# Kernel optimization log

Hardware: AMD Instinct MI355X
Metric: run time of the kernel (lower is better)

## Reference

```python
import jax, jax.numpy as jnp
import numpy as np

NUM_MIXTURES = 10
DIM_INPUT = 512
DIM_FEATURES = 512
SEQ_LEN = 512
BATCH = 16
NUM_CHAR = 1024
DIM_CONTEXT = 256


def setup_inputs() -> dict:
    key = jax.random.key(0)
    ks = jax.random.split(key, 6)
    inputs = jax.random.normal(ks[0], (SEQ_LEN, BATCH, DIM_INPUT), dtype=jnp.float32)
    context_vectors = jax.random.normal(ks[1], (NUM_CHAR, BATCH, DIM_CONTEXT), dtype=jnp.float32)
    init_means = jnp.zeros((BATCH, NUM_MIXTURES), dtype=jnp.float32)
    # StackedLinearLayers params: 2 layers, leaky_relu between, out dim = 3*K
    s1 = 1.0 / np.sqrt(DIM_INPUT)
    s2 = 1.0 / np.sqrt(DIM_FEATURES)
    W1 = jax.random.uniform(ks[2], (DIM_INPUT, DIM_FEATURES), jnp.float32, -s1, s1)
    b1 = jax.random.uniform(ks[3], (DIM_FEATURES,), jnp.float32, -s1, s1)
    W2 = jax.random.uniform(ks[4], (DIM_FEATURES, 3 * NUM_MIXTURES), jnp.float32, -s2, s2)
    b2 = jax.random.uniform(ks[5], (3 * NUM_MIXTURES,), jnp.float32, -s2, s2)
    return dict(inputs=inputs, context_vectors=context_vectors, init_means=init_means,
                W1=W1, b1=b1, W2=W2, b2=b2, extra_chars=0)


def reference(inputs, context_vectors, init_means, W1, b1, W2, b2, extra_chars):
    K = NUM_MIXTURES
    seq_len, batch, _ = inputs.shape
    num_char = context_vectors.shape[0]
    total_char = num_char + extra_chars

    # StackedLinearLayers: leaky_relu MLP, last layer linear -> (S, B, 3K)
    h = jax.nn.leaky_relu(inputs @ W1 + b1, negative_slope=0.01)
    outs = h @ W2 + b2
    outs = jax.nn.softplus(outs)  # pos_fun = softplus

    delta_means, vars_, weights = jnp.split(outs, 3, axis=2)  # each (S, B, K)
    delta_means = delta_means / 25.0
    vars_ = jnp.clip(vars_, 0.01, 100.0)
    means = jnp.cumsum(delta_means, axis=0) + init_means[None, :, :]  # (S, B, K)

    cidxs = jnp.arange(total_char, dtype=jnp.float32)  # (T,)
    # dists: (S, B, K, T)
    dists = -((means[..., None] - cidxs) ** 2) * vars_[..., None]
    # attn_weights = exp(logsumexp over mixtures)
    attn_weights = jnp.exp(
        jax.scipy.special.logsumexp(jnp.log(weights)[..., None] + dists, axis=2)
    )  # (S, B, T)

    # attended contexts: (S, B, D)
    attn_contexts = jnp.einsum('sbc,cbd->sbd', attn_weights[:, :, :num_char], context_vectors)
    return attn_contexts, attn_weights, means, vars_, weights
```

## Files before the change

### kernel.cpp

```cpp
#include <hip/hip_runtime.h>
#include <math.h>

#define S_LEN 512
#define BATCH 16
#define DIN   512
#define DF    512
#define NMIX  10
#define NCHAR 1024
#define DCTX  256
#define M_ROWS (S_LEN*BATCH)

#define OFF_CTXOUT 0
#define OFF_ATTN   (S_LEN*BATCH*DCTX)
#define OFF_MEANS  (OFF_ATTN + S_LEN*BATCH*NCHAR)
#define OFF_VARS   (OFF_MEANS + S_LEN*BATCH*NMIX)
#define OFF_WTS    (OFF_VARS  + S_LEN*BATCH*NMIX)

#define WS_XH    0
#define WS_W1T   (8u<<20)
#define WS_W2T   (9u<<20)
#define WS_HH    (10u<<20)
#define WS_ATTNH (26u<<20)
#define WS_BOUND (44u<<20)

#define NX4     1048576
#define CVT_BLOCKS (NX4/256)
#define W1T_BLOCKS 64
#define W2T_BLOCKS 64

typedef float    f32x16 __attribute__((ext_vector_type(16)));
typedef float    f32x4v __attribute__((ext_vector_type(4)));
typedef _Float16 f16x8  __attribute__((ext_vector_type(8)));

__device__ __forceinline__ unsigned short f2h(float x) {
    union { _Float16 h; unsigned short u; } cv;
    cv.h = (_Float16)x;
    return cv.u;
}
__device__ __forceinline__ ushort4 cvt4(float4 v) {
    ushort4 o; o.x = f2h(v.x); o.y = f2h(v.y); o.z = f2h(v.z); o.w = f2h(v.w);
    return o;
}
__device__ __forceinline__ void nt_store4(float* p, float a, float b, float c, float d) {
    f32x4v v; v.x = a; v.y = b; v.z = c; v.w = d;
    __builtin_nontemporal_store(v, (f32x4v*)p);
}

__global__ __launch_bounds__(256) void convert_kernel(
    const float* __restrict__ X, const float* __restrict__ W1,
    const float* __restrict__ W2,
    unsigned short* __restrict__ Xh, unsigned short* __restrict__ W1T,
    float* __restrict__ W2T, unsigned int* __restrict__ bound)
{
    const int bid = blockIdx.x;
    const int tid = threadIdx.x;
    if (bid < CVT_BLOCKS) {
        const int i4 = bid*256 + tid;
        ((ushort4*)Xh)[i4] = cvt4(((const float4*)X)[i4]);
    } else if (bid < CVT_BLOCKS + W1T_BLOCKS) {
        __shared__ unsigned short tile[64*68];
        const int b2 = bid - CVT_BLOCKS;
        const int k0 = (b2 >> 3) * 64, n0 = (b2 & 7) * 64;
        #pragma unroll
        for (int q = 0; q < 4; q++) {
            const int r = q*16 + (tid >> 4);
            const int c = (tid & 15) * 4;
            float4 v = *(const float4*)(W1 + (size_t)(k0+r)*DF + n0 + c);
            *(ushort4*)(tile + r*68 + c) = cvt4(v);
        }
        __syncthreads();
        #pragma unroll
        for (int q = 0; q < 4; q++) {
            const int n  = q*16 + (tid >> 4);
            const int kq = (tid & 15) * 4;
            ushort4 o;
            o.x = tile[(kq+0)*68 + n];
            o.y = tile[(kq+1)*68 + n];
            o.z = tile[(kq+2)*68 + n];
            o.w = tile[(kq+3)*68 + n];
            *(ushort4*)(W1T + (size_t)(n0+n)*DIN + k0 + kq) = o;
        }
    } else if (bid < CVT_BLOCKS + W1T_BLOCKS + W2T_BLOCKS) {
        const int idx = (bid - CVT_BLOCKS - W1T_BLOCKS)*256 + tid;
        if (idx < 512*32) {
            const int j = idx >> 9, k = idx & 511;
            W2T[idx] = (j < 30) ? W2[k*30 + j] : 0.f;
        }
    } else {
        if (tid < BATCH) bound[tid] = 0u;
    }
}

__global__ __launch_bounds__(256) void gemm1_kernel(
    const unsigned short* __restrict__ Xh, const unsigned short* __restrict__ W1T,
    const float* __restrict__ b1, unsigned short* __restrict__ Hh)
{
    __shared__ __align__(16) unsigned short As[64*72];
    __shared__ __align__(16) unsigned short Bs[64*72];
    const int row0 = (blockIdx.x >> 3) * 64;
    const int n0   = (blockIdx.x & 7)  * 64;
    const int tid  = threadIdx.x;
    const int lane = tid & 63, w = tid >> 6;
    const int wr = (w >> 1) * 32, wc = (w & 1) * 32;
    const int m  = lane & 31,  g  = lane >> 5;
    const int sa = tid >> 2,   ka = (tid & 3) * 16;

    f32x16 acc = {};
    const unsigned short* aptr = Xh  + (size_t)(row0+sa)*DIN + ka;
    const unsigned short* bptr = W1T + (size_t)(n0 +sa)*DIN + ka;

    for (int kt = 0; kt < DIN; kt += 64) {
        uint4 av0 = *(const uint4*)(aptr + kt);
        uint4 av1 = *(const uint4*)(aptr + kt + 8);
        uint4 bv0 = *(const uint4*)(bptr + kt);
        uint4 bv1 = *(const uint4*)(bptr + kt + 8);
        __syncthreads();
        *(uint4*)(As + sa*72 + ka)     = av0;
        *(uint4*)(As + sa*72 + ka + 8) = av1;
        *(uint4*)(Bs + sa*72 + ka)     = bv0;
        *(uint4*)(Bs + sa*72 + ka + 8) = bv1;
        __syncthreads();
        #pragma unroll
        for (int ks = 0; ks < 64; ks += 16) {
            f16x8 af = *(const f16x8*)(As + (wr+m)*72 + ks + g*8);
            f16x8 bf = *(const f16x8*)(Bs + (wc+m)*72 + ks + g*8);
            acc = __builtin_amdgcn_mfma_f32_32x32x16_f16(af, bf, acc, 0, 0, 0);
        }
    }
    const int ncol = n0 + wc + m;
    const float bb = b1[ncol];
    #pragma unroll
    for (int r = 0; r < 16; r++) {
        const int rowloc = (r & 3) + 8*(r >> 2) + 4*g;
        const int row = row0 + wr + rowloc;
        float v = acc[r] + bb;
        v = v > 0.f ? v : 0.01f * v;
        Hh[(size_t)row*DF + ncol] = f2h(v);
    }
}

__global__ __launch_bounds__(256) void gemm2_kernel(
    const unsigned short* __restrict__ Hh, const float* __restrict__ W2T,
    const float* __restrict__ b2,
    float* __restrict__ dmeans, float* __restrict__ dvars, float* __restrict__ dwts)
{
    __shared__ __align__(16) unsigned short Hs[32*520];
    const int tid = threadIdx.x;
    const int r0  = blockIdx.x * 32;
    {
        const uint4* src = (const uint4*)(Hh + (size_t)r0*DF);
        #pragma unroll
        for (int i = 0; i < 8; i++) {
            int u   = tid + i*256;
            int row = u >> 6;
            int col = (u & 63) * 8;
            *(uint4*)(Hs + row*520 + col) = src[u];
        }
    }
    __syncthreads();

    const int r  = tid & 31;
    const int j0 = tid >> 5;
    const unsigned short* hrow = Hs + r*520;
    float acc[4] = {0.f, 0.f, 0.f, 0.f};

    for (int k0 = 0; k0 < DF; k0 += 8) {
        union { uint4 u; _Float16 h[8]; } hv;
        hv.u = *(const uint4*)(hrow + k0);
        float wv[4][8];
        #pragma unroll
        for (int q = 0; q < 4; q++) {
            *(float4*)(wv[q])     = *(const float4*)(W2T + (size_t)(j0 + q*8)*DF + k0);
            *(float4*)(wv[q] + 4) = *(const float4*)(W2T + (size_t)(j0 + q*8)*DF + k0 + 4);
        }
        #pragma unroll
        for (int i = 0; i < 8; i++) {
            float hf = (float)hv.h[i];
            acc[0] = fmaf(hf, wv[0][i], acc[0]);
            acc[1] = fmaf(hf, wv[1][i], acc[1]);
            acc[2] = fmaf(hf, wv[2][i], acc[2]);
            acc[3] = fmaf(hf, wv[3][i], acc[3]);
        }
    }
    const int row = r0 + r;
    #pragma unroll
    for (int q = 0; q < 4; q++) {
        const int j = j0 + q*8;
        if (j >= 30) continue;
        float dot = acc[q] + b2[j];
        float sp  = fmaxf(dot, 0.f) + log1pf(__expf(-fabsf(dot)));
        if (j < 10)       dmeans[row*NMIX + j]      = sp / 25.0f;
        else if (j < 20)  dvars [row*NMIX + (j-10)] = fminf(fmaxf(sp, 0.01f), 100.f);
        else              dwts  [row*NMIX + (j-20)] = sp;
    }
}

__global__ __launch_bounds__(512) void scan_kernel(
    const float* __restrict__ init_means, float* __restrict__ means,
    const float* __restrict__ vars_g, unsigned int* __restrict__ bound)
{
    const int p    = blockIdx.x;
    const int s    = threadIdx.x;
    const int lane = s & 63;
    const int wid  = s >> 6;

    float x = means[s*(BATCH*NMIX) + p];
    #pragma unroll
    for (int d = 1; d < 64; d <<= 1) {
        float tv = __shfl_up(x, d, 64);
        if (lane >= d) x += tv;
    }
    __shared__ float wsum[8];
    __shared__ float wmax[8];
    if (lane == 63) wsum[wid] = x;
    __syncthreads();
    float off = init_means[p];
    for (int i = 0; i < wid; i++) off += wsum[i];
    x += off;
    means[s*(BATCH*NMIX) + p] = x;

    float v = vars_g[s*(BATCH*NMIX) + p];
    float reach = x + 4.8f * rsqrtf(v);
    #pragma unroll
    for (int d = 32; d >= 1; d >>= 1)
        reach = fmaxf(reach, __shfl_xor(reach, d, 64));
    if (lane == 0) wmax[wid] = reach;
    __syncthreads();
    if (s == 0) {
        float mx = wmax[0];
        #pragma unroll
        for (int i = 1; i < 8; i++) mx = fmaxf(mx, wmax[i]);
        atomicMax((int*)&bound[p / NMIX], __float_as_int(mx));
    }
}

__global__ __launch_bounds__(256) void attn_kernel(
    const float* __restrict__ means, const float* __restrict__ vars,
    const float* __restrict__ wts,   const unsigned int* __restrict__ bound,
    float* __restrict__ attn, unsigned short* __restrict__ attnh)
{
    const int row = blockIdx.x;
    const int b   = row & (BATCH-1);
    const int tid = threadIdx.x;
    const int bd  = (int)__int_as_float((int)bound[b]);
    const int kmax = min(NCHAR, (bd + 64) & ~63);
    const int t0  = tid * 4;

    float o[4] = {0.f, 0.f, 0.f, 0.f};
    if (t0 <= bd) {
        float m[NMIX], v[NMIX], w[NMIX];
        #pragma unroll
        for (int k = 0; k < NMIX; k++) {
            m[k] = means[row*NMIX + k];
            v[k] = vars [row*NMIX + k];
            w[k] = wts  [row*NMIX + k];
        }
        #pragma unroll
        for (int i = 0; i < 4; i++) {
            const float t = (float)(t0 + i);
            float sum = 0.f;
            #pragma unroll
            for (int k = 0; k < NMIX; k++) {
                float d = t - m[k];
                sum += w[k] * __expf(-d*d*v[k]);
            }
            o[i] = sum;
        }
    }
    nt_store4(attn + (size_t)row*NCHAR + t0, o[0], o[1], o[2], o[3]);
    if (t0 < kmax) {
        ushort4 h; h.x = f2h(o[0]); h.y = f2h(o[1]); h.z = f2h(o[2]); h.w = f2h(o[3]);
        *(ushort4*)(attnh + (size_t)row*NCHAR + t0) = h;
    }
}

__global__ __launch_bounds__(256) void ctx_mfma_kernel(
    const unsigned short* __restrict__ attnh, const float* __restrict__ ctx,
    const unsigned int* __restrict__ bound, float* __restrict__ out)
{
    __shared__ __align__(16) unsigned short As[64*72];
    __shared__ __align__(16) unsigned short Bs[64*72];
    const int bid  = blockIdx.x;
    const int b    = bid >> 5;
    const int rem  = bid & 31;
    const int s0   = (rem >> 2) * 64;
    const int d0   = (rem & 3)  * 64;
    const int tid  = threadIdx.x;
    const int lane = tid & 63, w = tid >> 6;
    const int wr = (w >> 1) * 32, wc = (w & 1) * 32;
    const int m  = lane & 31,  g  = lane >> 5;
    const int sl = tid >> 2,   tq = (tid & 3) * 16;
    const int tb = tid & 63,   db = (tid >> 6) * 16;

    const int bd   = (int)__int_as_float((int)bound[b]);
    const int kmax = min(NCHAR, (bd + 64) & ~63);

    f32x16 acc = {};
    const unsigned short* abase = attnh + (size_t)(s0+sl)*(BATCH*NCHAR) + b*NCHAR + tq;
    const float*          bbase = ctx   + (size_t)b*DCTX + d0 + db;

    for (int kt = 0; kt < kmax; kt += 64) {
        uint4 a0  = *(const uint4*)(abase + kt);
        uint4 a1  = *(const uint4*)(abase + kt + 8);
        float4 bf0 = *(const float4*)(bbase + (size_t)(kt+tb)*(BATCH*DCTX));
        float4 bf1 = *(const float4*)(bbase + (size_t)(kt+tb)*(BATCH*DCTX) + 4);
        float4 bf2 = *(const float4*)(bbase + (size_t)(kt+tb)*(BATCH*DCTX) + 8);
        float4 bf3 = *(const float4*)(bbase + (size_t)(kt+tb)*(BATCH*DCTX) + 12);
        __syncthreads();
        *(uint4*)(As + sl*72 + tq)     = a0;
        *(uint4*)(As + sl*72 + tq + 8) = a1;
        {
            ushort4 h0 = cvt4(bf0), h1 = cvt4(bf1), h2 = cvt4(bf2), h3 = cvt4(bf3);
            Bs[(db + 0)*72 + tb] = h0.x;  Bs[(db + 1)*72 + tb] = h0.y;
            Bs[(db + 2)*72 + tb] = h0.z;  Bs[(db + 3)*72 + tb] = h0.w;
            Bs[(db + 4)*72 + tb] = h1.x;  Bs[(db + 5)*72 + tb] = h1.y;
            Bs[(db + 6)*72 + tb] = h1.z;  Bs[(db + 7)*72 + tb] = h1.w;
            Bs[(db + 8)*72 + tb] = h2.x;  Bs[(db + 9)*72 + tb] = h2.y;
            Bs[(db +10)*72 + tb] = h2.z;  Bs[(db +11)*72 + tb] = h2.w;
            Bs[(db +12)*72 + tb] = h3.x;  Bs[(db +13)*72 + tb] = h3.y;
            Bs[(db +14)*72 + tb] = h3.z;  Bs[(db +15)*72 + tb] = h3.w;
        }
        __syncthreads();
        #pragma unroll
        for (int ks = 0; ks < 64; ks += 16) {
            f16x8 af = *(const f16x8*)(As + (wr+m)*72 + ks + g*8);
            f16x8 bf = *(const f16x8*)(Bs + (wc+m)*72 + ks + g*8);
            acc = __builtin_amdgcn_mfma_f32_32x32x16_f16(af, bf, acc, 0, 0, 0);
        }
    }
    #pragma unroll
    for (int r = 0; r < 16; r++) {
        int rowloc = (r & 3) + 8*(r >> 2) + 4*g;
        int s = s0 + wr + rowloc;
        __builtin_nontemporal_store(acc[r],
            out + (size_t)s*(BATCH*DCTX) + b*DCTX + d0 + wc + m);
    }
}

extern "C" void kernel_launch(void* const* d_in, const int* in_sizes, int n_in,
                              void* d_out, int out_size, void* d_ws, size_t ws_size,
                              hipStream_t stream)
{
    const float* X     = (const float*)d_in[0];
    const float* ctx   = (const float*)d_in[1];
    const float* initm = (const float*)d_in[2];
    const float* W1    = (const float*)d_in[3];
    const float* b1    = (const float*)d_in[4];
    const float* W2    = (const float*)d_in[5];
    const float* b2    = (const float*)d_in[6];

    float* out      = (float*)d_out;
    float* out_ctx  = out + OFF_CTXOUT;
    float* out_attn = out + OFF_ATTN;
    float* out_mean = out + OFF_MEANS;
    float* out_var  = out + OFF_VARS;
    float* out_wts  = out + OFF_WTS;

    char* ws = (char*)d_ws;
    unsigned short* Xh    = (unsigned short*)(ws + WS_XH);
    unsigned short* W1T   = (unsigned short*)(ws + WS_W1T);
    float*          W2T   = (float*)         (ws + WS_W2T);
    unsigned short* Hh    = (unsigned short*)(ws + WS_HH);
    unsigned short* attnh = (unsigned short*)(ws + WS_ATTNH);
    unsigned int*   bnd   = (unsigned int*)  (ws + WS_BOUND);

    convert_kernel<<<CVT_BLOCKS + W1T_BLOCKS + W2T_BLOCKS + 1, 256, 0, stream>>>(
        X, W1, W2, Xh, W1T, W2T, bnd);
    gemm1_kernel<<<(M_ROWS/64)*(DF/64), 256, 0, stream>>>(Xh, W1T, b1, Hh);
    gemm2_kernel<<<M_ROWS/32, 256, 0, stream>>>(Hh, W2T, b2, out_mean, out_var, out_wts);
    scan_kernel<<<BATCH*NMIX, 512, 0, stream>>>(initm, out_mean, out_var, bnd);
    attn_kernel<<<M_ROWS, 256, 0, stream>>>(out_mean, out_var, out_wts, bnd,
                                            out_attn, attnh);
    ctx_mfma_kernel<<<16*8*4, 256, 0, stream>>>(attnh, ctx, bnd, out_ctx);
}
```

Before: 142.8 us.

## Fuse conversion into GEMM1 and merge scan, attention and context into one kernel

Removes the standalone fp32-to-fp16 conversion pass. GEMM1 now converts X and W1 on the fly into XOR-swizzled LDS tiles, uses 64x128 tiles with two MFMA accumulators, and fills W2T from spare blocks. Scan, attention-weight generation and the context MFMA are merged into one kernel per (batch, 32-step) tile. That kernel recomputes the prefix sum of the means locally and computes a per-tile bound instead of the global per-batch atomic bound, so the fp16 attention buffer never goes to global memory and several launches are dropped. The cost is redundant prefix-scan work in each block and only 256 blocks of 512 threads, which may limit parallelism in the dominant stage.

```diff
diff --git a/kernel.cpp b/kernel.cpp
--- a/kernel.cpp
+++ b/kernel.cpp
@@ -16,17 +16,9 @@
 #define OFF_VARS   (OFF_MEANS + S_LEN*BATCH*NMIX)
 #define OFF_WTS    (OFF_VARS  + S_LEN*BATCH*NMIX)
 
-#define WS_XH    0
-#define WS_W1T   (8u<<20)
-#define WS_W2T   (9u<<20)
-#define WS_HH    (10u<<20)
-#define WS_ATTNH (26u<<20)
-#define WS_BOUND (44u<<20)
-
-#define NX4     1048576
-#define CVT_BLOCKS (NX4/256)
-#define W1T_BLOCKS 64
-#define W2T_BLOCKS 64
+#define WS_HH    0
+#define WS_W2T   (8u<<20)
+#define WS_DM    (9u<<20)
 
 typedef float    f32x16 __attribute__((ext_vector_type(16)));
 typedef float    f32x4v __attribute__((ext_vector_type(4)));
@@ -46,103 +38,97 @@
     __builtin_nontemporal_store(v, (f32x4v*)p);
 }
 
-__global__ __launch_bounds__(256) void convert_kernel(
+
+__global__ __launch_bounds__(256) void gemm1_kernel(
     const float* __restrict__ X, const float* __restrict__ W1,
-    const float* __restrict__ W2,
-    unsigned short* __restrict__ Xh, unsigned short* __restrict__ W1T,
-    float* __restrict__ W2T, unsigned int* __restrict__ bound)
+    const float* __restrict__ b1, unsigned short* __restrict__ Hh,
+    const float* __restrict__ W2, float* __restrict__ W2T)
 {
-    const int bid = blockIdx.x;
     const int tid = threadIdx.x;
-    if (bid < CVT_BLOCKS) {
-        const int i4 = bid*256 + tid;
-        ((ushort4*)Xh)[i4] = cvt4(((const float4*)X)[i4]);
-    } else if (bid < CVT_BLOCKS + W1T_BLOCKS) {
-        __shared__ unsigned short tile[64*68];
-        const int b2 = bid - CVT_BLOCKS;
-        const int k0 = (b2 >> 3) * 64, n0 = (b2 & 7) * 64;
-        #pragma unroll
-        for (int q = 0; q < 4; q++) {
-            const int r = q*16 + (tid >> 4);
-            const int c = (tid & 15) * 4;
-            float4 v = *(const float4*)(W1 + (size_t)(k0+r)*DF + n0 + c);
-            *(ushort4*)(tile + r*68 + c) = cvt4(v);
-        }
-        __syncthreads();
-        #pragma unroll
-        for (int q = 0; q < 4; q++) {
-            const int n  = q*16 + (tid >> 4);
-            const int kq = (tid & 15) * 4;
-            ushort4 o;
-            o.x = tile[(kq+0)*68 + n];
-            o.y = tile[(kq+1)*68 + n];
-            o.z = tile[(kq+2)*68 + n];
-            o.w = tile[(kq+3)*68 + n];
-            *(ushort4*)(W1T + (size_t)(n0+n)*DIN + k0 + kq) = o;
-        }
-    } else if (bid < CVT_BLOCKS + W1T_BLOCKS + W2T_BLOCKS) {
-        const int idx = (bid - CVT_BLOCKS - W1T_BLOCKS)*256 + tid;
-        if (idx < 512*32) {
+    if (blockIdx.x >= 512) {
+        const int base = (blockIdx.x - 512) * 4096 + tid;
+        #pragma unroll
+        for (int i = 0; i < 16; i++) {
+            const int idx = base + i*256;
             const int j = idx >> 9, k = idx & 511;
             W2T[idx] = (j < 30) ? W2[k*30 + j] : 0.f;
         }
-    } else {
-        if (tid < BATCH) bound[tid] = 0u;
-    }
-}
-
-__global__ __launch_bounds__(256) void gemm1_kernel(
-    const unsigned short* __restrict__ Xh, const unsigned short* __restrict__ W1T,
-    const float* __restrict__ b1, unsigned short* __restrict__ Hh)
-{
-    __shared__ __align__(16) unsigned short As[64*72];
-    __shared__ __align__(16) unsigned short Bs[64*72];
-    const int row0 = (blockIdx.x >> 3) * 64;
-    const int n0   = (blockIdx.x & 7)  * 64;
-    const int tid  = threadIdx.x;
+        return;
+    }
+    __shared__ __align__(16) unsigned short As[64*64];
+    __shared__ __align__(16) unsigned short Bs[128*64];
+    const int row0 = (blockIdx.x >> 2) * 64;
+    const int n0   = (blockIdx.x & 3)  * 128;
     const int lane = tid & 63, w = tid >> 6;
-    const int wr = (w >> 1) * 32, wc = (w & 1) * 32;
+    const int wr = (w >> 1) * 32, wc = (w & 1) * 64;
     const int m  = lane & 31,  g  = lane >> 5;
-    const int sa = tid >> 2,   ka = (tid & 3) * 16;
-
-    f32x16 acc = {};
-    const unsigned short* aptr = Xh  + (size_t)(row0+sa)*DIN + ka;
-    const unsigned short* bptr = W1T + (size_t)(n0 +sa)*DIN + ka;
+    const int sa = tid >> 2, ka = (tid & 3) * 16;
+    const int kb = tid & 63, nq = (tid >> 6) * 32;
+
+    f32x16 acc0 = {}, acc1 = {};
+    const float* aptr = X + (size_t)(row0 + sa)*DIN + ka;
+    const int sza = (sa & 7) << 3;
+    const int szm = (m  & 7) << 3;
 
     for (int kt = 0; kt < DIN; kt += 64) {
-        uint4 av0 = *(const uint4*)(aptr + kt);
-        uint4 av1 = *(const uint4*)(aptr + kt + 8);
-        uint4 bv0 = *(const uint4*)(bptr + kt);
-        uint4 bv1 = *(const uint4*)(bptr + kt + 8);
+        float4 a0 = *(const float4*)(aptr + kt + 0);
+        float4 a1 = *(const float4*)(aptr + kt + 4);
+        float4 a2 = *(const float4*)(aptr + kt + 8);
+        float4 a3 = *(const float4*)(aptr + kt + 12);
+        const float* bp = W1 + (size_t)(kt + kb)*DF + n0 + nq;
+        float4 bv[8];
+        #pragma unroll
+        for (int u = 0; u < 8; u++) bv[u] = *(const float4*)(bp + u*4);
         __syncthreads();
-        *(uint4*)(As + sa*72 + ka)     = av0;
-        *(uint4*)(As + sa*72 + ka + 8) = av1;
-        *(uint4*)(Bs + sa*72 + ka)     = bv0;
-        *(uint4*)(Bs + sa*72 + ka + 8) = bv1;
+        {
+            union { ushort4 h[4]; uint4 q[2]; } ta;
+            ta.h[0] = cvt4(a0); ta.h[1] = cvt4(a1);
+            ta.h[2] = cvt4(a2); ta.h[3] = cvt4(a3);
+            *(uint4*)(As + sa*64 + ( ka      ^ sza)) = ta.q[0];
+            *(uint4*)(As + sa*64 + ((ka + 8) ^ sza)) = ta.q[1];
+        }
+        {
+            const int cb = (kb & ~7), cs = (kb & 7);
+            #pragma unroll
+            for (int u = 0; u < 8; u++) {
+                ushort4 h = cvt4(bv[u]);
+                const int n = nq + u*4;
+                Bs[(n+0)*64 + (cb ^ (((n+0)&7)<<3)) + cs] = h.x;
+                Bs[(n+1)*64 + (cb ^ (((n+1)&7)<<3)) + cs] = h.y;
+                Bs[(n+2)*64 + (cb ^ (((n+2)&7)<<3)) + cs] = h.z;
+                Bs[(n+3)*64 + (cb ^ (((n+3)&7)<<3)) + cs] = h.w;
+            }
+        }
         __syncthreads();
         #pragma unroll
         for (int ks = 0; ks < 64; ks += 16) {
-            f16x8 af = *(const f16x8*)(As + (wr+m)*72 + ks + g*8);
-            f16x8 bf = *(const f16x8*)(Bs + (wc+m)*72 + ks + g*8);
-            acc = __builtin_amdgcn_mfma_f32_32x32x16_f16(af, bf, acc, 0, 0, 0);
-        }
-    }
-    const int ncol = n0 + wc + m;
-    const float bb = b1[ncol];
+            const int ac = ks + g*8;
+            f16x8 af  = *(const f16x8*)(As + (wr+m)*64      + (ac ^ szm));
+            f16x8 bf0 = *(const f16x8*)(Bs + (wc+m)*64      + (ac ^ szm));
+            f16x8 bf1 = *(const f16x8*)(Bs + (wc+32+m)*64   + (ac ^ szm));
+            acc0 = __builtin_amdgcn_mfma_f32_32x32x16_f16(af, bf0, acc0, 0, 0, 0);
+            acc1 = __builtin_amdgcn_mfma_f32_32x32x16_f16(af, bf1, acc1, 0, 0, 0);
+        }
+    }
+    const int nc0 = n0 + wc + m;
+    const float bb0 = b1[nc0], bb1 = b1[nc0 + 32];
     #pragma unroll
     for (int r = 0; r < 16; r++) {
         const int rowloc = (r & 3) + 8*(r >> 2) + 4*g;
         const int row = row0 + wr + rowloc;
-        float v = acc[r] + bb;
-        v = v > 0.f ? v : 0.01f * v;
-        Hh[(size_t)row*DF + ncol] = f2h(v);
+        float v0 = acc0[r] + bb0;
+        float v1 = acc1[r] + bb1;
+        v0 = v0 > 0.f ? v0 : 0.01f * v0;
+        v1 = v1 > 0.f ? v1 : 0.01f * v1;
+        Hh[(size_t)row*DF + nc0]      = f2h(v0);
+        Hh[(size_t)row*DF + nc0 + 32] = f2h(v1);
     }
 }
 
 __global__ __launch_bounds__(256) void gemm2_kernel(
     const unsigned short* __restrict__ Hh, const float* __restrict__ W2T,
     const float* __restrict__ b2,
-    float* __restrict__ dmeans, float* __restrict__ dvars, float* __restrict__ dwts)
+    float* __restrict__ dm_ws, float* __restrict__ dvars, float* __restrict__ dwts)
 {
     __shared__ __align__(16) unsigned short Hs[32*520];
     const int tid = threadIdx.x;
@@ -189,151 +175,147 @@
         if (j >= 30) continue;
         float dot = acc[q] + b2[j];
         float sp  = fmaxf(dot, 0.f) + log1pf(__expf(-fabsf(dot)));
-        if (j < 10)       dmeans[row*NMIX + j]      = sp / 25.0f;
-        else if (j < 20)  dvars [row*NMIX + (j-10)] = fminf(fmaxf(sp, 0.01f), 100.f);
-        else              dwts  [row*NMIX + (j-20)] = sp;
-    }
-}
-
-__global__ __launch_bounds__(512) void scan_kernel(
-    const float* __restrict__ init_means, float* __restrict__ means,
-    const float* __restrict__ vars_g, unsigned int* __restrict__ bound)
+        if (j < 10) {
+            const int bb = row & (BATCH-1), s = row >> 4;
+            dm_ws[((size_t)bb*NMIX + j)*S_LEN + s] = sp * (1.f/25.f);
+        }
+        else if (j < 20)  dvars[row*NMIX + (j-10)] = fminf(fmaxf(sp, 0.01f), 100.f);
+        else              dwts [row*NMIX + (j-20)] = sp;
+    }
+}
+
+__global__ __launch_bounds__(512) void fused_kernel(
+    const float* __restrict__ dm_ws, const float* __restrict__ init_means,
+    const float* __restrict__ vars_g, const float* __restrict__ wts_g,
+    const float* __restrict__ ctx,
+    float* __restrict__ means_out, float* __restrict__ attn_out,
+    float* __restrict__ ctxout)
 {
-    const int p    = blockIdx.x;
-    const int s    = threadIdx.x;
-    const int lane = s & 63;
-    const int wid  = s >> 6;
-
-    float x = means[s*(BATCH*NMIX) + p];
-    #pragma unroll
-    for (int d = 1; d < 64; d <<= 1) {
-        float tv = __shfl_up(x, d, 64);
-        if (lane >= d) x += tv;
-    }
-    __shared__ float wsum[8];
-    __shared__ float wmax[8];
-    if (lane == 63) wsum[wid] = x;
+    __shared__ float mlds[320];
+    __shared__ float vlds[320];
+    __shared__ float wlds[320];
+    __shared__ float redbuf[8];
+    __shared__ __align__(16) unsigned short As[32*64];
+    __shared__ __align__(16) unsigned short Bs[256*64];
+
+    const int bid = blockIdx.x;
+    const int b   = bid >> 4;
+    const int s0  = (bid & 15) * 32;
+    const int tid = threadIdx.x;
+    const int lane = tid & 63, w = tid >> 6;
+    const int m = lane & 31, g = lane >> 5;
+
+    const int send = s0 + 32;
+    for (int k = w; k < NMIX; k += 8) {
+        float carry = init_means[b*NMIX + k];
+        const float* chain = dm_ws + ((size_t)b*NMIX + k)*S_LEN;
+        for (int sseg = 0; sseg < send; sseg += 64) {
+            const int s = sseg + lane;
+            float v = (s < send) ? chain[s] : 0.f;
+            #pragma unroll
+            for (int d = 1; d < 64; d <<= 1) {
+                float t = __shfl_up(v, d, 64);
+                if (lane >= d) v += t;
+            }
+            const float x = v + carry;
+            carry = __shfl(x, 63, 64);
+            if (s >= s0 && s < send) mlds[(s - s0)*NMIX + k] = x;
+        }
+    }
+    if (tid < 320) {
+        const int s = tid / NMIX, k = tid - s*NMIX;
+        const int row = (s0 + s)*BATCH + b;
+        vlds[tid] = vars_g[row*NMIX + k];
+        wlds[tid] = wts_g [row*NMIX + k];
+    }
     __syncthreads();
-    float off = init_means[p];
-    for (int i = 0; i < wid; i++) off += wsum[i];
-    x += off;
-    means[s*(BATCH*NMIX) + p] = x;
-
-    float v = vars_g[s*(BATCH*NMIX) + p];
-    float reach = x + 4.8f * rsqrtf(v);
-    #pragma unroll
-    for (int d = 32; d >= 1; d >>= 1)
-        reach = fmaxf(reach, __shfl_xor(reach, d, 64));
-    if (lane == 0) wmax[wid] = reach;
+
+    float reach = 0.f;
+    if (tid < 320) {
+        const int s = tid / NMIX, k = tid - s*NMIX;
+        means_out[((s0 + s)*BATCH + b)*NMIX + k] = mlds[tid];
+        reach = mlds[tid] + 4.8f * rsqrtf(vlds[tid]);
+    }
+    #pragma unroll
+    for (int d = 32; d >= 1; d >>= 1) reach = fmaxf(reach, __shfl_xor(reach, d, 64));
+    if (lane == 0) redbuf[w] = reach;
     __syncthreads();
-    if (s == 0) {
-        float mx = wmax[0];
-        #pragma unroll
-        for (int i = 1; i < 8; i++) mx = fmaxf(mx, wmax[i]);
-        atomicMax((int*)&bound[p / NMIX], __float_as_int(mx));
-    }
-}
-
-__global__ __launch_bounds__(256) void attn_kernel(
-    const float* __restrict__ means, const float* __restrict__ vars,
-    const float* __restrict__ wts,   const unsigned int* __restrict__ bound,
-    float* __restrict__ attn, unsigned short* __restrict__ attnh)
-{
-    const int row = blockIdx.x;
-    const int b   = row & (BATCH-1);
-    const int tid = threadIdx.x;
-    const int bd  = (int)__int_as_float((int)bound[b]);
-    const int kmax = min(NCHAR, (bd + 64) & ~63);
-    const int t0  = tid * 4;
-
-    float o[4] = {0.f, 0.f, 0.f, 0.f};
-    if (t0 <= bd) {
-        float m[NMIX], v[NMIX], w[NMIX];
-        #pragma unroll
-        for (int k = 0; k < NMIX; k++) {
-            m[k] = means[row*NMIX + k];
-            v[k] = vars [row*NMIX + k];
-            w[k] = wts  [row*NMIX + k];
-        }
+    float rmax = redbuf[0];
+    #pragma unroll
+    for (int i = 1; i < 8; i++) rmax = fmaxf(rmax, redbuf[i]);
+    const int kmax = min(NCHAR, (((int)rmax) + 64) & ~63);
+
+    const int r  = tid >> 4;
+    const int ti = tid & 15;
+    float mr[NMIX], vr[NMIX], wr_[NMIX];
+    #pragma unroll
+    for (int k = 0; k < NMIX; k++) {
+        mr[k] = mlds[r*NMIX + k];
+        vr[k] = vlds[r*NMIX + k];
+        wr_[k] = wlds[r*NMIX + k];
+    }
+    const size_t arow = (size_t)((s0 + r)*BATCH + b) * NCHAR;
+
+    const int tb = tid & 63, dq = tid >> 6;
+    const float* cbase = ctx + (size_t)b*DCTX + dq*32;
+    const int szm = (m & 7) << 3;
+
+    f32x16 acc = {};
+    for (int kt = 0; kt < kmax; kt += 64) {
+        float o[4];
         #pragma unroll
         for (int i = 0; i < 4; i++) {
-            const float t = (float)(t0 + i);
+            const float t = (float)(kt + ti*4 + i);
             float sum = 0.f;
             #pragma unroll
             for (int k = 0; k < NMIX; k++) {
-                float d = t - m[k];
-                sum += w[k] * __expf(-d*d*v[k]);
+                float d = t - mr[k];
+                sum += wr_[k] * __expf(-d*d*vr[k]);
             }
             o[i] = sum;
         }
-    }
-    nt_store4(attn + (size_t)row*NCHAR + t0, o[0], o[1], o[2], o[3]);
-    if (t0 < kmax) {
-        ushort4 h; h.x = f2h(o[0]); h.y = f2h(o[1]); h.z = f2h(o[2]); h.w = f2h(o[3]);
-        *(ushort4*)(attnh + (size_t)row*NCHAR + t0) = h;
-    }
-}
-
-__global__ __launch_bounds__(256) void ctx_mfma_kernel(
-    const unsigned short* __restrict__ attnh, const float* __restrict__ ctx,
-    const unsigned int* __restrict__ bound, float* __restrict__ out)
-{
-    __shared__ __align__(16) unsigned short As[64*72];
-    __shared__ __align__(16) unsigned short Bs[64*72];
-    const int bid  = blockIdx.x;
-    const int b    = bid >> 5;
-    const int rem  = bid & 31;
-    const int s0   = (rem >> 2) * 64;
-    const int d0   = (rem & 3)  * 64;
-    const int tid  = threadIdx.x;
-    const int lane = tid & 63, w = tid >> 6;
-    const int wr = (w >> 1) * 32, wc = (w & 1) * 32;
-    const int m  = lane & 31,  g  = lane >> 5;
-    const int sl = tid >> 2,   tq = (tid & 3) * 16;
-    const int tb = tid & 63,   db = (tid >> 6) * 16;
-
-    const int bd   = (int)__int_as_float((int)bound[b]);
-    const int kmax = min(NCHAR, (bd + 64) & ~63);
-
-    f32x16 acc = {};
-    const unsigned short* abase = attnh + (size_t)(s0+sl)*(BATCH*NCHAR) + b*NCHAR + tq;
-    const float*          bbase = ctx   + (size_t)b*DCTX + d0 + db;
-
-    for (int kt = 0; kt < kmax; kt += 64) {
-        uint4 a0  = *(const uint4*)(abase + kt);
-        uint4 a1  = *(const uint4*)(abase + kt + 8);
-        float4 bf0 = *(const float4*)(bbase + (size_t)(kt+tb)*(BATCH*DCTX));
-        float4 bf1 = *(const float4*)(bbase + (size_t)(kt+tb)*(BATCH*DCTX) + 4);
-        float4 bf2 = *(const float4*)(bbase + (size_t)(kt+tb)*(BATCH*DCTX) + 8);
-        float4 bf3 = *(const float4*)(bbase + (size_t)(kt+tb)*(BATCH*DCTX) + 12);
+        float4 cf[8];
+        #pragma unroll
+        for (int u = 0; u < 8; u++)
+            cf[u] = *(const float4*)(cbase + (size_t)(kt + tb)*(BATCH*DCTX) + u*4);
         __syncthreads();
-        *(uint4*)(As + sl*72 + tq)     = a0;
-        *(uint4*)(As + sl*72 + tq + 8) = a1;
+        nt_store4(attn_out + arow + kt + ti*4, o[0], o[1], o[2], o[3]);
         {
-            ushort4 h0 = cvt4(bf0), h1 = cvt4(bf1), h2 = cvt4(bf2), h3 = cvt4(bf3);
-            Bs[(db + 0)*72 + tb] = h0.x;  Bs[(db + 1)*72 + tb] = h0.y;
-            Bs[(db + 2)*72 + tb] = h0.z;  Bs[(db + 3)*72 + tb] = h0.w;
-            Bs[(db + 4)*72 + tb] = h1.x;  Bs[(db + 5)*72 + tb] = h1.y;
-            Bs[(db + 6)*72 + tb] = h1.z;  Bs[(db + 7)*72 + tb] = h1.w;
-            Bs[(db + 8)*72 + tb] = h2.x;  Bs[(db + 9)*72 + tb] = h2.y;
-            Bs[(db +10)*72 + tb] = h2.z;  Bs[(db +11)*72 + tb] = h2.w;
-            Bs[(db +12)*72 + tb] = h3.x;  Bs[(db +13)*72 + tb] = h3.y;
-            Bs[(db +14)*72 + tb] = h3.z;  Bs[(db +15)*72 + tb] = h3.w;
+            ushort4 h; h.x = f2h(o[0]); h.y = f2h(o[1]); h.z = f2h(o[2]); h.w = f2h(o[3]);
+            const int c = ti*4;
+            *(ushort4*)(As + r*64 + ((c & ~7) ^ ((r&7)<<3)) + (c & 7)) = h;
+        }
+        {
+            const int cb = (tb & ~7), cs = (tb & 7);
+            #pragma unroll
+            for (int u = 0; u < 8; u++) {
+                ushort4 h = cvt4(cf[u]);
+                const int n = dq*32 + u*4;
+                Bs[(n+0)*64 + (cb ^ (((n+0)&7)<<3)) + cs] = h.x;
+                Bs[(n+1)*64 + (cb ^ (((n+1)&7)<<3)) + cs] = h.y;
+                Bs[(n+2)*64 + (cb ^ (((n+2)&7)<<3)) + cs] = h.z;
+                Bs[(n+3)*64 + (cb ^ (((n+3)&7)<<3)) + cs] = h.w;
+            }
         }
         __syncthreads();
         #pragma unroll
         for (int ks = 0; ks < 64; ks += 16) {
-            f16x8 af = *(const f16x8*)(As + (wr+m)*72 + ks + g*8);
-            f16x8 bf = *(const f16x8*)(Bs + (wc+m)*72 + ks + g*8);
+            const int ac = ks + g*8;
+            f16x8 af = *(const f16x8*)(As + m*64 + (ac ^ szm));
+            const int brow = w*32 + m;
+            f16x8 bf = *(const f16x8*)(Bs + brow*64 + (ac ^ ((brow&7)<<3)));
             acc = __builtin_amdgcn_mfma_f32_32x32x16_f16(af, bf, acc, 0, 0, 0);
         }
     }
-    #pragma unroll
-    for (int r = 0; r < 16; r++) {
-        int rowloc = (r & 3) + 8*(r >> 2) + 4*g;
-        int s = s0 + wr + rowloc;
-        __builtin_nontemporal_store(acc[r],
-            out + (size_t)s*(BATCH*DCTX) + b*DCTX + d0 + wc + m);
+    for (int t = kmax + ti*4; t < NCHAR; t += 64)
+        nt_store4(attn_out + arow + t, 0.f, 0.f, 0.f, 0.f);
+
+    #pragma unroll
+    for (int rr = 0; rr < 16; rr++) {
+        const int rowloc = (rr & 3) + 8*(rr >> 2) + 4*g;
+        const int s = s0 + rowloc;
+        __builtin_nontemporal_store(acc[rr],
+            ctxout + ((size_t)s*BATCH + b)*DCTX + w*32 + m);
     }
 }
 
@@ -357,19 +339,12 @@
     float* out_wts  = out + OFF_WTS;
 
     char* ws = (char*)d_ws;
-    unsigned short* Xh    = (unsigned short*)(ws + WS_XH);
-    unsigned short* W1T   = (unsigned short*)(ws + WS_W1T);
-    float*          W2T   = (float*)         (ws + WS_W2T);
-    unsigned short* Hh    = (unsigned short*)(ws + WS_HH);
-    unsigned short* attnh = (unsigned short*)(ws + WS_ATTNH);
-    unsigned int*   bnd   = (unsigned int*)  (ws + WS_BOUND);
-
-    convert_kernel<<<CVT_BLOCKS + W1T_BLOCKS + W2T_BLOCKS + 1, 256, 0, stream>>>(
-        X, W1, W2, Xh, W1T, W2T, bnd);
-    gemm1_kernel<<<(M_ROWS/64)*(DF/64), 256, 0, stream>>>(Xh, W1T, b1, Hh);
-    gemm2_kernel<<<M_ROWS/32, 256, 0, stream>>>(Hh, W2T, b2, out_mean, out_var, out_wts);
-    scan_kernel<<<BATCH*NMIX, 512, 0, stream>>>(initm, out_mean, out_var, bnd);
-    attn_kernel<<<M_ROWS, 256, 0, stream>>>(out_mean, out_var, out_wts, bnd,
-                                            out_attn, attnh);
-    ctx_mfma_kernel<<<16*8*4, 256, 0, stream>>>(attnh, ctx, bnd, out_ctx);
-}
+    unsigned short* Hh   = (unsigned short*)(ws + WS_HH);
+    float*          W2T  = (float*)         (ws + WS_W2T);
+    float*          dmws = (float*)         (ws + WS_DM);
+
+    gemm1_kernel<<<512 + 4, 256, 0, stream>>>(X, W1, b1, Hh, W2, W2T);
+    gemm2_kernel<<<M_ROWS/32, 256, 0, stream>>>(Hh, W2T, b2, dmws, out_var, out_wts);
+    fused_kernel<<<BATCH*16, 512, 0, stream>>>(dmws, initm, out_var, out_wts, ctx,
+                                               out_mean, out_attn, out_ctx);
+}
```

Measured after the change: 149.7 us. 1.05x slower.
